# Optimization experiments

Measured on AMD Instinct MI355X. Metric: run time of the kernel, lower is better.

## Reference

```python
import jax, jax.numpy as jnp
import numpy as np

B, N, D, H = 4, 2048, 256, 8
DK = D // H
SCALE = np.sqrt(DK).astype(np.float32)


def setup_inputs() -> dict:
    key = jax.random.key(0)
    ks = jax.random.split(key, 8)
    s = 1.0 / np.sqrt(D)
    return {
        "x": jax.random.normal(ks[0], (B, N, D), jnp.float32),
        "edge_weights": jax.random.normal(ks[1], (B, N, N), jnp.float32),
        "mask": jax.random.randint(ks[2], (B, N, N), 0, 2, jnp.int32),
        "w_q": jax.random.normal(ks[3], (D, D), jnp.float32) * s,
        "w_k": jax.random.normal(ks[4], (D, D), jnp.float32) * s,
        "w_v": jax.random.normal(ks[5], (D, D), jnp.float32) * s,
        "w_o": jax.random.normal(ks[6], (D, D), jnp.float32) * s,
        "b_o": jax.random.normal(ks[7], (D,), jnp.float32) * s,
    }


def reference(x, edge_weights, mask, w_q, w_k, w_v, w_o, b_o):
    # torch Linear: y = x @ W.T ; split into heads -> [B, H, N, DK]
    def split_heads(t):
        return t.reshape(B, N, H, DK).transpose(0, 2, 1, 3)

    Q = split_heads(x @ w_q.T)
    K = split_heads(x @ w_k.T)
    V = split_heads(x @ w_v.T)

    scores = jnp.einsum("bhnd,bhmd->bhnm", Q, K) / SCALE
    scores = scores + edge_weights[:, None, :, :]
    scores = jnp.where(mask[:, None, :, :] == 0, jnp.float32(-1e9), scores)
    attn = jax.nn.softmax(scores, axis=-1)  # dropout is identity in eval
    out = jnp.einsum("bhnm,bhmd->bhnd", attn, V)
    out = out.transpose(0, 2, 1, 3).reshape(B, N, D)
    return out @ w_o.T + b_o
```

## Files before the change

### kernel.cpp

```cpp
#include <hip/hip_runtime.h>

#define LOG2E 1.4426950408889634f
#define NEGBIG -3.0e38f

typedef float  f32x4  __attribute__((ext_vector_type(4)));
typedef float  f32x16 __attribute__((ext_vector_type(16)));
typedef short  bf16x8 __attribute__((ext_vector_type(8)));
typedef unsigned short u16x4 __attribute__((ext_vector_type(4)));
typedef int    i32x4  __attribute__((ext_vector_type(4)));
typedef unsigned int u32x2 __attribute__((ext_vector_type(2)));

__device__ __forceinline__ unsigned short f2bf(float f) {
  union { float f; unsigned u; } v; v.f = f;
  unsigned r = v.u + 0x7FFFu + ((v.u >> 16) & 1u);
  return (unsigned short)(r >> 16);
}

__device__ __forceinline__ unsigned cvtpk(float a, float b) {
  unsigned r;
  asm("v_cvt_pk_bf16_f32 %0, %1, %2" : "=v"(r) : "v"(a), "v"(b));
  return r;
}

__device__ __forceinline__ bf16x8 load_cvt8(const float* p) {
  f32x4 a = *(const f32x4*)p;
  f32x4 b = *(const f32x4*)(p + 4);
  bf16x8 r;
  r[0]=(short)f2bf(a[0]); r[1]=(short)f2bf(a[1]); r[2]=(short)f2bf(a[2]); r[3]=(short)f2bf(a[3]);
  r[4]=(short)f2bf(b[0]); r[5]=(short)f2bf(b[1]); r[6]=(short)f2bf(b[2]); r[7]=(short)f2bf(b[3]);
  return r;
}

__global__ __launch_bounds__(256) void qkv_kernel(
    const float* __restrict__ x,
    const float* __restrict__ wq, const float* __restrict__ wk, const float* __restrict__ wv,
    const float* __restrict__ wo,
    unsigned short* __restrict__ Qo, unsigned short* __restrict__ Ko,
    unsigned short* __restrict__ Vto, unsigned short* __restrict__ woF)
{
  const int mode = blockIdx.y;
  if (mode == 3) {
    const int e = (blockIdx.x*256 + threadIdx.x) * 2;
    const int wv_ = e >> 13;
    const int ks  = (e >> 10) & 7;
    const int df  = (e >> 9) & 1;
    const int lp  = (e >> 3) & 63;
    const int j   = e & 7;
    const int row = wv_*32 + df*16 + (lp & 15);
    const int col = ks*32 + (lp >> 4)*8 + j;
    const float a0 = wo[(size_t)row*256 + col];
    const float a1 = wo[(size_t)row*256 + col + 1];
    woF[e]     = f2bf(a0);
    woF[e + 1] = f2bf(a1);
    return;
  }
  const int n0   = blockIdx.x * 64;
  const int b    = n0 >> 11;
  const int nl0  = n0 & 2047;
  const int wave = threadIdx.x >> 6;
  const int lane = threadIdx.x & 63;
  const int li = lane & 15, qt = lane >> 4;

  f32x4 acc[4][4];
#pragma unroll
  for (int i = 0; i < 4; i++)
#pragma unroll
    for (int j = 0; j < 4; j++) acc[i][j] = (f32x4)0.0f;

  if (mode < 2) {
    const float* w = mode ? wk : wq;
    const float osc = mode ? 1.0f : (1.4426950408889634f / 5.656854249492381f);
#pragma unroll
    for (int ks = 0; ks < 8; ks++) {
      bf16x8 af[4], bfr[4];
#pragma unroll
      for (int dm = 0; dm < 4; dm++)
        af[dm] = load_cvt8(w + (size_t)(wave*64 + dm*16 + li)*256 + ks*32 + qt*8);
#pragma unroll
      for (int nf = 0; nf < 4; nf++)
        bfr[nf] = load_cvt8(x + (size_t)(n0 + nf*16 + li)*256 + ks*32 + qt*8);
#pragma unroll
      for (int dm = 0; dm < 4; dm++)
#pragma unroll
        for (int nf = 0; nf < 4; nf++)
          acc[dm][nf] = __builtin_amdgcn_mfma_f32_16x16x32_bf16(af[dm], bfr[nf], acc[dm][nf], 0, 0, 0);
    }
#pragma unroll
    for (int dm = 0; dm < 4; dm++) {
      const int dbase = wave*64 + dm*16 + qt*4;
      const int h = dbase >> 5, dk = dbase & 31;
#pragma unroll
      for (int nf = 0; nf < 4; nf++) {
        const int nl = nl0 + nf*16 + li;
        u16x4 o;
#pragma unroll
        for (int r = 0; r < 4; r++) o[r] = f2bf(acc[dm][nf][r] * osc);
        if (mode == 0) {
          *(u16x4*)(Qo + ((size_t)(b*8 + h)*2048 + nl)*32 + dk) = o;
        } else {
          const size_t addr = (size_t)(b*8 + h)*65536
              + (size_t)(nl >> 5)*1024 + (size_t)((dk >> 4) & 1)*512
              + (size_t)((nl & 31) + 32*((dk >> 3) & 1))*8 + (dk & 7);
          *(u16x4*)(Ko + addr) = o;
        }
      }
    }
  } else {
#pragma unroll
    for (int ks = 0; ks < 8; ks++) {
      bf16x8 af[4], bfr[4];
#pragma unroll
      for (int nm = 0; nm < 4; nm++)
        af[nm] = load_cvt8(x + (size_t)(n0 + nm*16 + li)*256 + ks*32 + qt*8);
#pragma unroll
      for (int df = 0; df < 4; df++)
        bfr[df] = load_cvt8(wv + (size_t)(wave*64 + df*16 + li)*256 + ks*32 + qt*8);
#pragma unroll
      for (int nm = 0; nm < 4; nm++)
#pragma unroll
        for (int df = 0; df < 4; df++)
          acc[nm][df] = __builtin_amdgcn_mfma_f32_16x16x32_bf16(af[nm], bfr[df], acc[nm][df], 0, 0, 0);
    }
#pragma unroll
    for (int nm = 0; nm < 4; nm++) {
      const int nl = nl0 + nm*16 + qt*4;
#pragma unroll
      for (int df = 0; df < 4; df++) {
        const int d = wave*64 + df*16 + li;
        const int h = d >> 5, dv = d & 31;
        u16x4 o;
#pragma unroll
        for (int r = 0; r < 4; r++) o[r] = f2bf(acc[nm][df][r]);
        const size_t addr = (size_t)(b*8 + h)*65536
            + (size_t)(nl >> 5)*1024 + (size_t)((nl >> 4) & 1)*512
            + (size_t)(((nl >> 3) & 1)*32 + dv)*8 + (nl & 7);
        *(u16x4*)(Vto + addr) = o;
      }
    }
  }
}

__global__ __launch_bounds__(512, 2) void attn_kernel(
    const unsigned short* __restrict__ Qg,
    const unsigned short* __restrict__ Kf,
    const unsigned short* __restrict__ Vf,
    const float* __restrict__ edge,
    const int*   __restrict__ mask,
    const unsigned short* __restrict__ woF,
    const float* __restrict__ bo,
    float* __restrict__ Y)
{
  __shared__ __attribute__((aligned(16))) float me_s[2][4096];
  __shared__ __attribute__((aligned(16))) unsigned short o_lds[32][264];

  const int bid = blockIdx.x;
  const int b  = (bid >> 1) & 3;
  const int qi = ((bid >> 3) << 1) | (bid & 1);
  const int q0 = qi * 32;
  const int tid  = threadIdx.x;
  const int wave = tid >> 6;
  const int lane = tid & 63;
  const int ql = lane & 31, hi = lane >> 5;
  const int h = wave;

  const unsigned short* qbase = Qg + ((size_t)(b*8 + h)*2048 + q0)*32;
  const unsigned short* kf = Kf + (size_t)(b*8 + h)*65536 + lane*8;
  const unsigned short* vf = Vf + (size_t)(b*8 + h)*65536 + lane*8;

  const int q_s = tid >> 4;
  const int k4  = (tid & 15) * 4;
  const float* eaddr = edge + ((size_t)b*2048 + q0 + q_s)*2048 + k4;
  const int*   maddr = mask + ((size_t)b*2048 + q0 + q_s)*2048 + k4;
  const int sC2  = (((k4 & 31) >> 3) * 2) + ((k4 >> 2) & 1);
  const int widx = (k4 >> 5)*1024 + (sC2*32 + (q_s ^ sC2))*4;
  int rix[4];
#pragma unroll
  for (int rg = 0; rg < 4; rg++) {
    const int C2 = rg*2 + hi;
    rix[rg] = (C2*32 + (ql ^ C2)) * 4;
  }

  const bf16x8 qf0 = *(const bf16x8*)(qbase + (size_t)ql*32 +  0 + hi*8);
  const bf16x8 qf1 = *(const bf16x8*)(qbase + (size_t)ql*32 + 16 + hi*8);

  {
    f32x4 e0 = *(const f32x4*)eaddr;
    i32x4 m0 = *(const i32x4*)maddr;
    f32x4 e1 = *(const f32x4*)(eaddr + 64);
    i32x4 m1 = *(const i32x4*)(maddr + 64);
    f32x4 v0, v1;
#pragma unroll
    for (int r = 0; r < 4; r++) v0[r] = m0[r] ? e0[r]*LOG2E : NEGBIG;
#pragma unroll
    for (int r = 0; r < 4; r++) v1[r] = m1[r] ? e1[r]*LOG2E : NEGBIG;
    *(f32x4*)&me_s[0][widx] = v0;
    *(f32x4*)&me_s[0][widx + 2048] = v1;
  }
  __syncthreads();

  f32x4 se0 = *(const f32x4*)(eaddr + 128);
  i32x4 sm0 = *(const i32x4*)(maddr + 128);
  f32x4 se1 = *(const f32x4*)(eaddr + 192);
  i32x4 sm1 = *(const i32x4*)(maddr + 192);

  bf16x8 kXa = *(const bf16x8*)(kf);
  bf16x8 kXb = *(const bf16x8*)(kf + 512);
  bf16x8 kYa, kYb;

  float lsum = 0.f;
  f32x16 oacc0 = (f32x16)0.0f;
  f32x16 oacc1 = (f32x16)0.0f;

  union CU { f32x16 v; f32x4 q[4]; };

#define PV_KS(SV, HALF, VA, OA)                                               \
  {                                                                           \
    unsigned a0 = cvtpk(SV[(HALF)*8+0], SV[(HALF)*8+1]);                      \
    unsigned a1 = cvtpk(SV[(HALF)*8+2], SV[(HALF)*8+3]);                      \
    unsigned b0 = cvtpk(SV[(HALF)*8+4], SV[(HALF)*8+5]);                      \
    unsigned b1 = cvtpk(SV[(HALF)*8+6], SV[(HALF)*8+7]);                      \
    u32x2 p0 = __builtin_amdgcn_permlane32_swap(a0, b0, false, false);        \
    u32x2 p1 = __builtin_amdgcn_permlane32_swap(a1, b1, false, false);        \
    i32x4 pw4;                                                                \
    pw4[0] = (int)p0[0]; pw4[1] = (int)p1[0];                                 \
    pw4[2] = (int)p0[1]; pw4[3] = (int)p1[1];                                 \
    const bf16x8 pf = __builtin_bit_cast(bf16x8, pw4);                        \
    OA = __builtin_amdgcn_mfma_f32_32x32x16_bf16(VA, pf, OA, 0, 0, 0);        \
  }

#define GROUP(KB, T, KCa, KCb, KNa, KNb)                                      \
  {                                                                           \
    const size_t nxt = (size_t)(((KB) + 1) & 63) * 1024;                      \
    KNa = *(const bf16x8*)(kf + nxt);                                         \
    KNb = *(const bf16x8*)(kf + nxt + 512);                                   \
    const bf16x8 vA0 = *(const bf16x8*)(vf + (size_t)(KB)*1024);              \
    const bf16x8 vA1 = *(const bf16x8*)(vf + (size_t)(KB)*1024 + 512);        \
    CU c;                                                                     \
    _Pragma("unroll")                                                         \
    for (int rg = 0; rg < 4; rg++)                                            \
      c.q[rg] = *(const f32x4*)(mb + (T)*1024 + rix[rg]);                     \
    f32x16 s = __builtin_amdgcn_mfma_f32_32x32x16_bf16(KCa, qf0, c.v, 0, 0, 0); \
    s = __builtin_amdgcn_mfma_f32_32x32x16_bf16(KCb, qf1, s, 0, 0, 0);        \
    _Pragma("unroll")                                                         \
    for (int i = 0; i < 16; i++) s[i] = __builtin_amdgcn_exp2f(s[i]);         \
    {                                                                         \
      float r0 = 0.f, r1 = 0.f, r2 = 0.f, r3 = 0.f;                           \
      _Pragma("unroll")                                                       \
      for (int i = 0; i < 4; i++) {                                           \
        r0 += s[4*i]; r1 += s[4*i+1]; r2 += s[4*i+2]; r3 += s[4*i+3];         \
      }                                                                       \
      lsum += (r0 + r1) + (r2 + r3);                                          \
    }                                                                         \
    PV_KS(s, 0, vA0, oacc0)                                                   \
    PV_KS(s, 1, vA1, oacc1)                                                   \
  }

  for (int p = 0; p < 16; ++p) {
    const float* mb = &me_s[p & 1][0];
    if (p < 15) {
      f32x4 v0, v1;
#pragma unroll
      for (int r = 0; r < 4; r++) v0[r] = sm0[r] ? se0[r]*LOG2E : NEGBIG;
#pragma unroll
      for (int r = 0; r < 4; r++) v1[r] = sm1[r] ? se1[r]*LOG2E : NEGBIG;
      *(f32x4*)&me_s[(p + 1) & 1][widx] = v0;
      *(f32x4*)&me_s[(p + 1) & 1][widx + 2048] = v1;
    }
    if (p < 14) {
      se0 = *(const f32x4*)(eaddr + (p + 2)*128);
      sm0 = *(const i32x4*)(maddr + (p + 2)*128);
      se1 = *(const f32x4*)(eaddr + (p + 2)*128 + 64);
      sm1 = *(const i32x4*)(maddr + (p + 2)*128 + 64);
    }
    const int g0 = p * 4;
    GROUP(g0,     0, kXa, kXb, kYa, kYb)
    GROUP(g0 + 1, 1, kYa, kYb, kXa, kXb)
    GROUP(g0 + 2, 2, kXa, kXb, kYa, kYb)
    GROUP(g0 + 3, 3, kYa, kYb, kXa, kXb)
    __syncthreads();
  }
#undef GROUP
#undef PV_KS

  {
    const f32x16 oacc = oacc0 + oacc1;
    const float ltot = lsum + __shfl_xor(lsum, 32);
    const float rl = 1.0f / ltot;
#pragma unroll
    for (int rg = 0; rg < 4; rg++) {
      u16x4 o;
#pragma unroll
      for (int r = 0; r < 4; r++) o[r] = f2bf(oacc[rg*4 + r] * rl);
      *(u16x4*)&o_lds[ql][h*32 + rg*8 + hi*4] = o;
    }
  }
  __syncthreads();

  {
    const int li = lane & 15, qt = lane >> 4;
    const unsigned short* wof = woF + wave*8192 + lane*8;
    f32x4 acc2[2][2];
#pragma unroll
    for (int i = 0; i < 2; i++)
#pragma unroll
      for (int j = 0; j < 2; j++) acc2[i][j] = (f32x4)0.0f;
#pragma unroll
    for (int ks = 0; ks < 8; ks++) {
      const bf16x8 af0 = *(const bf16x8*)(wof + ks*1024);
      const bf16x8 af1 = *(const bf16x8*)(wof + ks*1024 + 512);
      const bf16x8 b0 = *(const bf16x8*)&o_lds[li][ks*32 + qt*8];
      const bf16x8 b1 = *(const bf16x8*)&o_lds[16 + li][ks*32 + qt*8];
      acc2[0][0] = __builtin_amdgcn_mfma_f32_16x16x32_bf16(af0, b0, acc2[0][0], 0, 0, 0);
      acc2[0][1] = __builtin_amdgcn_mfma_f32_16x16x32_bf16(af0, b1, acc2[0][1], 0, 0, 0);
      acc2[1][0] = __builtin_amdgcn_mfma_f32_16x16x32_bf16(af1, b0, acc2[1][0], 0, 0, 0);
      acc2[1][1] = __builtin_amdgcn_mfma_f32_16x16x32_bf16(af1, b1, acc2[1][1], 0, 0, 0);
    }
#pragma unroll
    for (int df = 0; df < 2; df++) {
      const int d0 = wave*32 + df*16 + qt*4;
      const f32x4 bo4 = *(const f32x4*)(bo + d0);
#pragma unroll
      for (int nf = 0; nf < 2; nf++) {
        const int n = nf*16 + li;
        f32x4 y = acc2[df][nf] + bo4;
        *(f32x4*)(Y + ((size_t)(b*2048 + q0 + n))*256 + d0) = y;
      }
    }
  }
}

extern "C" void kernel_launch(void* const* d_in, const int* in_sizes, int n_in,
                              void* d_out, int out_size, void* d_ws, size_t ws_size,
                              hipStream_t stream) {
  const float* x  = (const float*)d_in[0];
  const float* ew = (const float*)d_in[1];
  const int*   mk = (const int*)d_in[2];
  const float* wq = (const float*)d_in[3];
  const float* wk = (const float*)d_in[4];
  const float* wv = (const float*)d_in[5];
  const float* wo = (const float*)d_in[6];
  const float* bo = (const float*)d_in[7];
  float* y = (float*)d_out;

  unsigned short* Q   = (unsigned short*)d_ws;
  unsigned short* Kf  = Q  + 2097152;
  unsigned short* Vf  = Kf + 2097152;
  unsigned short* woF = Vf + 2097152;

  qkv_kernel<<<dim3(128, 4), 256, 0, stream>>>(x, wq, wk, wv, wo, Q, Kf, Vf, woF);
  attn_kernel<<<256, 512, 0, stream>>>(Q, Kf, Vf, ew, mk, woF, bo, y);
}
```

Measured before the change: 81.20 us.

## Load edge/mask directly into MFMA accumulator layout, drop LDS staging

```diff
diff --git a/kernel.cpp b/kernel.cpp
--- a/kernel.cpp
+++ b/kernel.cpp
@@ -150,7 +150,6 @@
     const float* __restrict__ bo,
     float* __restrict__ Y)
 {
-  __shared__ __attribute__((aligned(16))) float me_s[2][4096];
   __shared__ __attribute__((aligned(16))) unsigned short o_lds[32][264];
 
   const int bid = blockIdx.x;
@@ -166,42 +165,11 @@
   const unsigned short* qbase = Qg + ((size_t)(b*8 + h)*2048 + q0)*32;
   const unsigned short* kf = Kf + (size_t)(b*8 + h)*65536 + lane*8;
   const unsigned short* vf = Vf + (size_t)(b*8 + h)*65536 + lane*8;
-
-  const int q_s = tid >> 4;
-  const int k4  = (tid & 15) * 4;
-  const float* eaddr = edge + ((size_t)b*2048 + q0 + q_s)*2048 + k4;
-  const int*   maddr = mask + ((size_t)b*2048 + q0 + q_s)*2048 + k4;
-  const int sC2  = (((k4 & 31) >> 3) * 2) + ((k4 >> 2) & 1);
-  const int widx = (k4 >> 5)*1024 + (sC2*32 + (q_s ^ sC2))*4;
-  int rix[4];
-#pragma unroll
-  for (int rg = 0; rg < 4; rg++) {
-    const int C2 = rg*2 + hi;
-    rix[rg] = (C2*32 + (ql ^ C2)) * 4;
-  }
+  const float* erow = edge + ((size_t)b*2048 + q0 + ql)*2048 + hi*4;
+  const int*   mrow = mask + ((size_t)b*2048 + q0 + ql)*2048 + hi*4;
 
   const bf16x8 qf0 = *(const bf16x8*)(qbase + (size_t)ql*32 +  0 + hi*8);
   const bf16x8 qf1 = *(const bf16x8*)(qbase + (size_t)ql*32 + 16 + hi*8);
-
-  {
-    f32x4 e0 = *(const f32x4*)eaddr;
-    i32x4 m0 = *(const i32x4*)maddr;
-    f32x4 e1 = *(const f32x4*)(eaddr + 64);
-    i32x4 m1 = *(const i32x4*)(maddr + 64);
-    f32x4 v0, v1;
-#pragma unroll
-    for (int r = 0; r < 4; r++) v0[r] = m0[r] ? e0[r]*LOG2E : NEGBIG;
-#pragma unroll
-    for (int r = 0; r < 4; r++) v1[r] = m1[r] ? e1[r]*LOG2E : NEGBIG;
-    *(f32x4*)&me_s[0][widx] = v0;
-    *(f32x4*)&me_s[0][widx + 2048] = v1;
-  }
-  __syncthreads();
-
-  f32x4 se0 = *(const f32x4*)(eaddr + 128);
-  i32x4 sm0 = *(const i32x4*)(maddr + 128);
-  f32x4 se1 = *(const f32x4*)(eaddr + 192);
-  i32x4 sm1 = *(const i32x4*)(maddr + 192);
 
   bf16x8 kXa = *(const bf16x8*)(kf);
   bf16x8 kXb = *(const bf16x8*)(kf + 512);
@@ -228,17 +196,22 @@
     OA = __builtin_amdgcn_mfma_f32_32x32x16_bf16(VA, pf, OA, 0, 0, 0);        \
   }
 
-#define GROUP(KB, T, KCa, KCb, KNa, KNb)                                      \
+#define GROUP(KB, KCa, KCb, KNa, KNb)                                         \
   {                                                                           \
-    const size_t nxt = (size_t)(((KB) + 1) & 63) * 1024;                      \
+    const int nxt = (((KB) + 1) & 63) * 1024;                                 \
     KNa = *(const bf16x8*)(kf + nxt);                                         \
     KNb = *(const bf16x8*)(kf + nxt + 512);                                   \
-    const bf16x8 vA0 = *(const bf16x8*)(vf + (size_t)(KB)*1024);              \
-    const bf16x8 vA1 = *(const bf16x8*)(vf + (size_t)(KB)*1024 + 512);        \
+    const bf16x8 vA0 = *(const bf16x8*)(vf + (KB)*1024);                      \
+    const bf16x8 vA1 = *(const bf16x8*)(vf + (KB)*1024 + 512);                \
     CU c;                                                                     \
     _Pragma("unroll")                                                         \
-    for (int rg = 0; rg < 4; rg++)                                            \
-      c.q[rg] = *(const f32x4*)(mb + (T)*1024 + rix[rg]);                     \
+    for (int rg = 0; rg < 4; rg++) {                                          \
+      const f32x4 e = *(const f32x4*)(erow + (KB)*32 + rg*8);                 \
+      const i32x4 m = *(const i32x4*)(mrow + (KB)*32 + rg*8);                 \
+      _Pragma("unroll")                                                       \
+      for (int r = 0; r < 4; r++)                                             \
+        c.q[rg][r] = m[r] ? e[r]*LOG2E : NEGBIG;                              \
+    }                                                                         \
     f32x16 s = __builtin_amdgcn_mfma_f32_32x32x16_bf16(KCa, qf0, c.v, 0, 0, 0); \
     s = __builtin_amdgcn_mfma_f32_32x32x16_bf16(KCb, qf1, s, 0, 0, 0);        \
     _Pragma("unroll")                                                         \
@@ -255,29 +228,11 @@
     PV_KS(s, 1, vA1, oacc1)                                                   \
   }
 
-  for (int p = 0; p < 16; ++p) {
-    const float* mb = &me_s[p & 1][0];
-    if (p < 15) {
-      f32x4 v0, v1;
-#pragma unroll
-      for (int r = 0; r < 4; r++) v0[r] = sm0[r] ? se0[r]*LOG2E : NEGBIG;
-#pragma unroll
-      for (int r = 0; r < 4; r++) v1[r] = sm1[r] ? se1[r]*LOG2E : NEGBIG;
-      *(f32x4*)&me_s[(p + 1) & 1][widx] = v0;
-      *(f32x4*)&me_s[(p + 1) & 1][widx + 2048] = v1;
-    }
-    if (p < 14) {
-      se0 = *(const f32x4*)(eaddr + (p + 2)*128);
-      sm0 = *(const i32x4*)(maddr + (p + 2)*128);
-      se1 = *(const f32x4*)(eaddr + (p + 2)*128 + 64);
-      sm1 = *(const i32x4*)(maddr + (p + 2)*128 + 64);
-    }
-    const int g0 = p * 4;
-    GROUP(g0,     0, kXa, kXb, kYa, kYb)
-    GROUP(g0 + 1, 1, kYa, kYb, kXa, kXb)
-    GROUP(g0 + 2, 2, kXa, kXb, kYa, kYb)
-    GROUP(g0 + 3, 3, kYa, kYb, kXa, kXb)
-    __syncthreads();
+  for (int t = 0; t < 64; t += 4) {
+    GROUP(t,     kXa, kXb, kYa, kYb)
+    GROUP(t + 1, kYa, kYb, kXa, kXb)
+    GROUP(t + 2, kXa, kXb, kYa, kYb)
+    GROUP(t + 3, kYa, kYb, kXa, kXb)
   }
 #undef GROUP
 #undef PV_KS
```

Measured after the change: 174.3 us. 115% more time.
